# Performance work log

Measured on AMD Instinct MI355X. Metric: run time of the kernel, lower is better.

## Reference

```python
import jax, jax.numpy as jnp
import numpy as np

NUM_INPUTS = 4096
NUM_LEAVES = 2048
BATCH = 16384


def setup_inputs() -> dict:
    key = jax.random.key(0)
    kx, ka = jax.random.split(key)
    x = jax.random.normal(kx, (BATCH, NUM_INPUTS), dtype=jnp.float32)
    hard_assignment = jax.random.randint(ka, (NUM_LEAVES,), 0, NUM_INPUTS, dtype=jnp.int64)
    return {"x": x, "hard_assignment": hard_assignment}


def reference(x, hard_assignment):
    # torch: x @ P_hard.T where P_hard[leaf, hard_assignment[leaf]] = 1.
    # A one-hot selection matmul is exactly a column gather of x:
    # out[b, leaf] = x[b, hard_assignment[leaf]]
    return jnp.take(x, hard_assignment, axis=1)  # [BATCH, NUM_LEAVES]
```

## Files before the change

kernel.cpp:

```cpp
#include <hip/hip_runtime.h>

#define NUM_INPUTS 4096
#define NUM_LEAVES 2048
#define ROWS_PER_BLOCK 2
#define BLK 256

typedef const __attribute__((address_space(1))) void* gas_ptr;
typedef __attribute__((address_space(3))) void* las_ptr;

__global__ __launch_bounds__(BLK) void FrozenInputToLeaf_gather2(
    const float* __restrict__ x,
    const int* __restrict__ idx,
    float* __restrict__ out) {
    __shared__ float rows[ROWS_PER_BLOCK][NUM_INPUTS];

    const int t = threadIdx.x;
    const size_t b0 = (size_t)blockIdx.x * ROWS_PER_BLOCK;

    const int4* __restrict__ iv = (const int4*)idx;
    const int4 i0 = iv[t * 2 + 0];
    const int4 i1 = iv[t * 2 + 1];

#pragma unroll
    for (int r = 0; r < ROWS_PER_BLOCK; ++r) {
        const float* __restrict__ src = x + (b0 + r) * NUM_INPUTS;
#pragma unroll
        for (int j = 0; j < 4; ++j) {
            const int e = (j * BLK + threadIdx.x) * 4;
            __builtin_amdgcn_global_load_lds((gas_ptr)(src + e),
                                             (las_ptr)(&rows[r][e]), 16, 0, 0);
        }
    }
    __syncthreads();

#pragma unroll
    for (int r = 0; r < ROWS_PER_BLOCK; ++r) {
        float4 o0, o1;
        o0.x = rows[r][i0.x];
        o0.y = rows[r][i0.y];
        o0.z = rows[r][i0.z];
        o0.w = rows[r][i0.w];
        o1.x = rows[r][i1.x];
        o1.y = rows[r][i1.y];
        o1.z = rows[r][i1.z];
        o1.w = rows[r][i1.w];

        float4* __restrict__ ov = (float4*)(out + (b0 + r) * NUM_LEAVES);
        ov[t * 2 + 0] = o0;
        ov[t * 2 + 1] = o1;
    }
}

extern "C" void kernel_launch(void* const* d_in, const int* in_sizes, int n_in,
                              void* d_out, int out_size, void* d_ws, size_t ws_size,
                              hipStream_t stream) {
    const float* x = (const float*)d_in[0];
    const int* idx = (const int*)d_in[1];
    float* out = (float*)d_out;

    const int batch = in_sizes[0] / NUM_INPUTS;
    const int grid = batch / ROWS_PER_BLOCK;

    FrozenInputToLeaf_gather2<<<grid, BLK, 0, stream>>>(x, idx, out);
}
```

Before: 74.48 us.

## Pipeline row loads through double-buffered LDS in single-wave blocks

Replaces 256-thread blocks that load two rows, then barrier, then gather, with 64-thread single-wave blocks that each process eight rows. Each block prefetches the next row into a second LDS buffer with global_load_lds while it gathers the current one, and uses explicit vmcnt waits instead of __syncthreads. The intent is to overlap HBM loads with LDS gathers and stores, and to drop block-level barriers. The cost is fewer resident waves per CU, since each 64-thread block still holds 32KB of LDS, and a vmcnt scheme that also counts global stores, which makes the waits more conservative.

```diff
diff --git a/kernel.cpp b/kernel.cpp
--- a/kernel.cpp
+++ b/kernel.cpp
@@ -2,52 +2,64 @@
 
 #define NUM_INPUTS 4096
 #define NUM_LEAVES 2048
-#define ROWS_PER_BLOCK 2
-#define BLK 256
+#define ROWS_PER_BLOCK 8
+#define BLK 64
 
 typedef const __attribute__((address_space(1))) void* gas_ptr;
 typedef __attribute__((address_space(3))) void* las_ptr;
 
-__global__ __launch_bounds__(BLK) void FrozenInputToLeaf_gather2(
+__global__ __launch_bounds__(BLK) void FrozenInputToLeaf_wavepipe(
     const float* __restrict__ x,
     const int* __restrict__ idx,
     float* __restrict__ out) {
-    __shared__ float rows[ROWS_PER_BLOCK][NUM_INPUTS];
+    __shared__ float buf[2][NUM_INPUTS];
 
-    const int t = threadIdx.x;
-    const size_t b0 = (size_t)blockIdx.x * ROWS_PER_BLOCK;
+    const int lane = threadIdx.x;
+    const size_t row0 = (size_t)blockIdx.x * ROWS_PER_BLOCK;
 
     const int4* __restrict__ iv = (const int4*)idx;
-    const int4 i0 = iv[t * 2 + 0];
-    const int4 i1 = iv[t * 2 + 1];
+    int4 ireg[8];
+#pragma unroll
+    for (int j = 0; j < 8; ++j) ireg[j] = iv[j * 64 + lane];
+
+    {
+        const float* __restrict__ src = x + row0 * NUM_INPUTS;
+#pragma unroll
+        for (int i = 0; i < 16; ++i) {
+            const int e = (i * 64 + lane) * 4;
+            __builtin_amdgcn_global_load_lds((gas_ptr)(src + e),
+                                             (las_ptr)(&buf[0][e]), 16, 0, 0);
+        }
+    }
 
 #pragma unroll
     for (int r = 0; r < ROWS_PER_BLOCK; ++r) {
-        const float* __restrict__ src = x + (b0 + r) * NUM_INPUTS;
+        const int p = r & 1;
+        if (r + 1 < ROWS_PER_BLOCK) {
+            const float* __restrict__ src = x + (row0 + r + 1) * NUM_INPUTS;
 #pragma unroll
-        for (int j = 0; j < 4; ++j) {
-            const int e = (j * BLK + threadIdx.x) * 4;
-            __builtin_amdgcn_global_load_lds((gas_ptr)(src + e),
-                                             (las_ptr)(&rows[r][e]), 16, 0, 0);
+            for (int i = 0; i < 16; ++i) {
+                const int e = (i * 64 + lane) * 4;
+                __builtin_amdgcn_global_load_lds((gas_ptr)(src + e),
+                                                 (las_ptr)(&buf[p ^ 1][e]), 16, 0, 0);
+            }
+            asm volatile("s_waitcnt vmcnt(16)" ::: "memory");
+        } else {
+            asm volatile("s_waitcnt vmcnt(0)" ::: "memory");
         }
-    }
-    __syncthreads();
+        __builtin_amdgcn_sched_barrier(0);
 
+        const float* __restrict__ cur = buf[p];
+        float4* __restrict__ ov = (float4*)(out + (row0 + r) * NUM_LEAVES);
 #pragma unroll
-    for (int r = 0; r < ROWS_PER_BLOCK; ++r) {
-        float4 o0, o1;
-        o0.x = rows[r][i0.x];
-        o0.y = rows[r][i0.y];
-        o0.z = rows[r][i0.z];
-        o0.w = rows[r][i0.w];
-        o1.x = rows[r][i1.x];
-        o1.y = rows[r][i1.y];
-        o1.z = rows[r][i1.z];
-        o1.w = rows[r][i1.w];
-
-        float4* __restrict__ ov = (float4*)(out + (b0 + r) * NUM_LEAVES);
-        ov[t * 2 + 0] = o0;
-        ov[t * 2 + 1] = o1;
+        for (int j = 0; j < 8; ++j) {
+            float4 v;
+            v.x = cur[ireg[j].x];
+            v.y = cur[ireg[j].y];
+            v.z = cur[ireg[j].z];
+            v.w = cur[ireg[j].w];
+            ov[j * 64 + lane] = v;
+        }
     }
 }
 
@@ -61,5 +73,5 @@
     const int batch = in_sizes[0] / NUM_INPUTS;
     const int grid = batch / ROWS_PER_BLOCK;
 
-    FrozenInputToLeaf_gather2<<<grid, BLK, 0, stream>>>(x, idx, out);
+    FrozenInputToLeaf_wavepipe<<<grid, BLK, 0, stream>>>(x, idx, out);
 }
```

After: 84.45 us. +13.4%, slower.

## Double-buffer row loads in LDS with explicit vmcnt waits across 8 rows per block

Applied to the files above, without the earlier changes.

Each block now handles 8 rows instead of 2, using two LDS row buffers. While the current row is gathered and written out, the next row is prefetched into the other buffer with global_load_lds. Hand-placed s_waitcnt vmcnt counts and raw s_barrier calls replace __syncthreads, so prefetch overlaps with the gather and store inside a block. In exchange the grid is four times smaller, leaving fewer independent blocks to hide latency, and correctness depends on the exact vmcnt bookkeeping of loads and stores.

```diff
diff --git a/kernel.cpp b/kernel.cpp
--- a/kernel.cpp
+++ b/kernel.cpp
@@ -2,52 +2,72 @@
 
 #define NUM_INPUTS 4096
 #define NUM_LEAVES 2048
-#define ROWS_PER_BLOCK 2
+#define R_PB 8
 #define BLK 256
 
 typedef const __attribute__((address_space(1))) void* gas_ptr;
 typedef __attribute__((address_space(3))) void* las_ptr;
+typedef float vfloat4 __attribute__((ext_vector_type(4)));
 
-__global__ __launch_bounds__(BLK) void FrozenInputToLeaf_gather2(
+__global__ __launch_bounds__(BLK) void FrozenInputToLeaf_pipe(
     const float* __restrict__ x,
     const int* __restrict__ idx,
     float* __restrict__ out) {
-    __shared__ float rows[ROWS_PER_BLOCK][NUM_INPUTS];
+    __shared__ float buf[2][NUM_INPUTS];
 
     const int t = threadIdx.x;
-    const size_t b0 = (size_t)blockIdx.x * ROWS_PER_BLOCK;
+    const size_t row0 = (size_t)blockIdx.x * R_PB;
 
     const int4* __restrict__ iv = (const int4*)idx;
     const int4 i0 = iv[t * 2 + 0];
     const int4 i1 = iv[t * 2 + 1];
 
-#pragma unroll
-    for (int r = 0; r < ROWS_PER_BLOCK; ++r) {
-        const float* __restrict__ src = x + (b0 + r) * NUM_INPUTS;
+    {
+        const float* __restrict__ src = x + row0 * NUM_INPUTS;
 #pragma unroll
         for (int j = 0; j < 4; ++j) {
-            const int e = (j * BLK + threadIdx.x) * 4;
+            const int e = (j * BLK + t) * 4;
             __builtin_amdgcn_global_load_lds((gas_ptr)(src + e),
-                                             (las_ptr)(&rows[r][e]), 16, 0, 0);
+                                             (las_ptr)(&buf[0][e]), 16, 0, 0);
         }
     }
-    __syncthreads();
 
 #pragma unroll
-    for (int r = 0; r < ROWS_PER_BLOCK; ++r) {
-        float4 o0, o1;
-        o0.x = rows[r][i0.x];
-        o0.y = rows[r][i0.y];
-        o0.z = rows[r][i0.z];
-        o0.w = rows[r][i0.w];
-        o1.x = rows[r][i1.x];
-        o1.y = rows[r][i1.y];
-        o1.z = rows[r][i1.z];
-        o1.w = rows[r][i1.w];
+    for (int r = 0; r < R_PB; ++r) {
+        const int p = r & 1;
+        if (r + 1 < R_PB) {
+            const float* __restrict__ src = x + (row0 + r + 1) * NUM_INPUTS;
+#pragma unroll
+            for (int j = 0; j < 4; ++j) {
+                const int e = (j * BLK + t) * 4;
+                __builtin_amdgcn_global_load_lds((gas_ptr)(src + e),
+                                                 (las_ptr)(&buf[p ^ 1][e]), 16, 0, 0);
+            }
+        }
+        if (r == 0)             asm volatile("s_waitcnt vmcnt(4)" ::: "memory");
+        else if (r + 1 < R_PB)  asm volatile("s_waitcnt vmcnt(6)" ::: "memory");
+        else                    asm volatile("s_waitcnt vmcnt(2)" ::: "memory");
+        __builtin_amdgcn_sched_barrier(0);
+        __builtin_amdgcn_s_barrier();
 
-        float4* __restrict__ ov = (float4*)(out + (b0 + r) * NUM_LEAVES);
+        const float* __restrict__ cur = buf[p];
+        vfloat4 o0, o1;
+        o0.x = cur[i0.x];
+        o0.y = cur[i0.y];
+        o0.z = cur[i0.z];
+        o0.w = cur[i0.w];
+        o1.x = cur[i1.x];
+        o1.y = cur[i1.y];
+        o1.z = cur[i1.z];
+        o1.w = cur[i1.w];
+
+        vfloat4* __restrict__ ov = (vfloat4*)(out + (row0 + r) * NUM_LEAVES);
         ov[t * 2 + 0] = o0;
         ov[t * 2 + 1] = o1;
+
+        asm volatile("s_waitcnt lgkmcnt(0)" ::: "memory");
+        __builtin_amdgcn_sched_barrier(0);
+        __builtin_amdgcn_s_barrier();
     }
 }
 
@@ -59,7 +79,7 @@
     float* out = (float*)d_out;
 
     const int batch = in_sizes[0] / NUM_INPUTS;
-    const int grid = batch / ROWS_PER_BLOCK;
+    const int grid = batch / R_PB;
 
-    FrozenInputToLeaf_gather2<<<grid, BLK, 0, stream>>>(x, idx, out);
+    FrozenInputToLeaf_pipe<<<grid, BLK, 0, stream>>>(x, idx, out);
 }
```

New measurement: 80.84 us. +8.5%, slower.
